# Kernel tuning notes

Hardware: AMD Instinct MI355X
Metric: run time of the kernel (lower is better)

## Reference

```python
import jax, jax.numpy as jnp
import numpy as np

DA, DZ, HID, IM = 5, 10, 128, 64


def _encode(x, w1, b1, w2, b2, w3, b3, wd, bd):
    # Conv2D k=4 s=2 'same' (pad 1,1) + ReLU, x3, then flatten + Dense(20)
    dn = ('NHWC', 'HWIO', 'NHWC')
    for w, b in ((w1, b1), (w2, b2), (w3, b3)):
        x = jax.lax.conv_general_dilated(x, w, (2, 2), [(1, 1), (1, 1)], dimension_numbers=dn)
        x = jax.nn.relu(x + b)
    x = x.reshape(x.shape[0], -1)
    return x @ wd + bd


def _lstm(a_in, k, rk, b):
    # keras LSTM, gate order i,f,c,o; stateful step-by-step == scan over shifted seq
    B = a_in.shape[0]
    def step(carry, x):
        h, c = carry
        g = x @ k + h @ rk + b
        gi, gf, gg, go = jnp.split(g, 4, axis=-1)
        c = jax.nn.sigmoid(gf) * c + jax.nn.sigmoid(gi) * jnp.tanh(gg)
        h = jax.nn.sigmoid(go) * jnp.tanh(c)
        return (h, c), h
    z = jnp.zeros((B, HID), a_in.dtype)
    _, hs = jax.lax.scan(step, (z, z), jnp.swapaxes(a_in, 0, 1))
    return hs  # [T, B, HID]


def _forward(images, w1, b1, w2, b2, w3, b3, wd, bd, lk, lrk, lb, wabc, babc):
    B, T = images.shape[0], images.shape[1]
    # encode all frames in one batched pass (per-frame encode is recursion-independent)
    lat = _encode(images.reshape(B * T, IM, IM, 1), w1, b1, w2, b2, w3, b3, wd, bd)
    a_all = lat[:, :DA].reshape(B, T, DA)  # encode() mean split
    # LSTM consumes a_prev: a0=zeros at t=0, then a_{t-1}
    a_in = jnp.concatenate([jnp.zeros((B, 1, DA), a_all.dtype), a_all[:, :-1]], axis=1)
    hs = _lstm(a_in, lk, lrk, lb)  # [T,B,HID]
    abc = hs @ wabc + babc  # [T,B,DZ*DZ+DA*DZ]
    A = abc[..., :DZ * DZ].reshape(T, B, DZ, DZ)
    C = abc[..., DZ * DZ:].reshape(T, B, DA, DZ)

    Q = 0.08 * jnp.eye(DZ, dtype=a_all.dtype)
    R = 0.03 * jnp.eye(DA, dtype=a_all.dtype)
    I = jnp.eye(DZ, dtype=a_all.dtype)
    std_min = 1e-4 * I

    def kf(carry, inp):
        z, P = carry
        At, Ct, at = inp
        z_hat = jnp.einsum('bij,bj->bi', At, z)
        P_hat = At @ P @ jnp.swapaxes(At, -1, -2) + Q
        resid = at - jnp.einsum('bij,bj->bi', Ct, z_hat)
        S = Ct @ P_hat @ jnp.swapaxes(Ct, -1, -2) + R
        K = P_hat @ jnp.swapaxes(Ct, -1, -2) @ jnp.linalg.inv(S)
        pz = z_hat + jnp.einsum('bij,bj->bi', K, resid)
        pP = (I - K @ Ct) @ P_hat
        # note: clamped P_hat is stored, but update() above used the unclamped one
        return (pz, pP), (z_hat, jnp.maximum(P_hat, std_min), pz, pP)

    z0 = jnp.zeros((B, DZ), a_all.dtype)
    P0 = jnp.broadcast_to(I, (B, DZ, DZ))
    _, (z_hat_s, P_hat_s, pz_s, pP_s) = jax.lax.scan(kf, (z0, P0), (A, C, jnp.swapaxes(a_all, 0, 1)))
    last_z, last_P = pz_s[-1], pP_s[-1]

    def rts(carry, inp):
        zs, Ps = carry
        pz_prev, pP_prev, Aj, zhj, Phj = inp
        D = pP_prev @ jnp.swapaxes(Aj, -1, -2) @ jnp.linalg.inv(Phj)
        zn = pz_prev + jnp.einsum('bij,bj->bi', D, zs - zhj)
        Pn = pP_prev + D @ (Ps - Phj) @ jnp.swapaxes(D, -1, -2)
        return (zn, Pn), (zn, Pn)

    # j = T-1 .. 1, reading post[j-1], A[j], z_hat[j], P_hat_clamped[j]
    rev = (pz_s[:-1][::-1], pP_s[:-1][::-1], A[1:][::-1], z_hat_s[1:][::-1], P_hat_s[1:][::-1])
    _, (zsm_r, Psm_r) = jax.lax.scan(rts, (last_z, last_P), rev)
    z_smooth = jnp.swapaxes(zsm_r[::-1], 0, 1)  # [B, T-1, DZ]
    P_smooth = jnp.swapaxes(Psm_r[::-1], 0, 1)  # [B, T-1, DZ, DZ]
    return z_smooth, P_smooth, a_all, A, C, last_z, last_P


def setup_inputs() -> dict:
    key = jax.random.key(0)
    ks = jax.random.split(key, 9)
    B, T = 3, 128
    f = lambda k, shape, s: jax.random.normal(k, shape, jnp.float32) * s
    return {
        'images': jax.random.uniform(ks[0], (B, T, IM, IM, 1), jnp.float32),
        'w1': f(ks[1], (4, 4, 1, 64), 0.25), 'b1': jnp.zeros((64,), jnp.float32),
        'w2': f(ks[2], (4, 4, 64, 128), 0.03), 'b2': jnp.zeros((128,), jnp.float32),
        'w3': f(ks[3], (4, 4, 128, 512), 0.022), 'b3': jnp.zeros((512,), jnp.float32),
        'wd': f(ks[4], (8 * 8 * 512, 20), 0.006), 'bd': jnp.zeros((20,), jnp.float32),
        'lk': f(ks[5], (DA, 4 * HID), 0.3), 'lrk': f(ks[6], (HID, 4 * HID), 0.08),
        'lb': jnp.zeros((4 * HID,), jnp.float32),
        'wabc': f(ks[7], (HID, DZ * DZ + DA * DZ), 0.02),
        'babc': jnp.zeros((DZ * DZ + DA * DZ,), jnp.float32),
    }


def reference(images, w1, b1, w2, b2, w3, b3, wd, bd, lk, lrk, lb, wabc, babc):
    return _forward(images, w1, b1, w2, b2, w3, b3, wd, bd, lk, lrk, lb, wabc, babc)
```

## Files before the change

kernel.cpp:

```cpp
#include <hip/hip_runtime.h>
#include <math.h>

typedef unsigned int   u32;
typedef unsigned short u16;
typedef short bf16x8 __attribute__((ext_vector_type(8)));
typedef float f32x4  __attribute__((ext_vector_type(4)));

#define OUT_ZS    0
#define OUT_PS    3810
#define OUT_AALL  41910
#define OUT_A     43830
#define OUT_C     82230
#define OUT_LASTZ 101430
#define OUT_LASTP 101460

__device__ __forceinline__ float sigm(float x){ return 1.f/(1.f+expf(-x)); }
__device__ __forceinline__ float safed(float d){
    return (fabsf(d) < 1e-30f) ? ((d < 0.f) ? -1e-30f : 1e-30f) : d;
}
__device__ __forceinline__ u16 f2b(float f) {
    union { float f; u32 u; } v; v.f = f;
    u32 r = v.u + 0x7fffu + ((v.u >> 16) & 1u);
    return (u16)(r >> 16);
}
__device__ __forceinline__ float b2f(u16 u) {
    union { u32 x; float f; } v; v.x = ((u32)u) << 16; return v.f;
}
__device__ __forceinline__ u32 packb(float a, float b){ return (u32)f2b(a) | ((u32)f2b(b) << 16); }

__device__ u16   r14_c1[25165824];
__device__ u16   r14_c2[12582912];
__device__ float r14_c3[12582912];
__device__ u16   r14_w2h[131072];
__device__ u16   r14_w2l[131072];
__device__ u16   r14_w3h[1048576];
__device__ u16   r14_w3l[1048576];
__device__ float r14_wdT[163840];
__device__ float r14_hs[49152];
__device__ float r14_zhat[3840];
__device__ float r14_phat[38400];
__device__ float r14_pz[3840];
__device__ float r14_pp[38400];
__device__ float r14_aall[1920];
__device__ float r14_A[38400];
__device__ float r14_C[19200];
__device__ float r14_G[38400];

__global__ __launch_bounds__(256) void conv1_r14(const float* __restrict__ img,
        const float* __restrict__ w1, const float* __restrict__ b1, u16* __restrict__ out)
{
    __shared__ float in_lds[66*66];
    const int f = blockIdx.x, tid = threadIdx.x;
    const int og = tid >> 5, sg = tid & 31;

    for (int i = tid; i < 66*66; i += 256) in_lds[i] = 0.f;
    __syncthreads();
    const float4* src = (const float4*)(img + f*4096);
    for (int i = tid; i < 1024; i += 256) {
        int r = i >> 4, c0 = (i & 15) * 4;
        float4 v = src[i];
        float* dst = &in_lds[(r+1)*66 + c0 + 1];
        dst[0]=v.x; dst[1]=v.y; dst[2]=v.z; dst[3]=v.w;
    }
    float wr[16][8];
    #pragma unroll
    for (int k = 0; k < 16; k++) {
        float4 a = *(const float4*)&w1[k*64 + og*8];
        float4 b = *(const float4*)&w1[k*64 + og*8 + 4];
        wr[k][0]=a.x; wr[k][1]=a.y; wr[k][2]=a.z; wr[k][3]=a.w;
        wr[k][4]=b.x; wr[k][5]=b.y; wr[k][6]=b.z; wr[k][7]=b.w;
    }
    float bias[8];
    #pragma unroll
    for (int j = 0; j < 8; j++) bias[j] = b1[og*8+j];
    __syncthreads();

    for (int yy = 0; yy < 32; yy++) {
        float inv[16];
        #pragma unroll
        for (int ky = 0; ky < 4; ky++)
            #pragma unroll
            for (int kx = 0; kx < 4; kx++)
                inv[ky*4+kx] = in_lds[(2*yy+ky)*66 + 2*sg+kx];
        float acc[8];
        #pragma unroll
        for (int j = 0; j < 8; j++) acc[j] = bias[j];
        #pragma unroll
        for (int k = 0; k < 16; k++)
            #pragma unroll
            for (int j = 0; j < 8; j++) acc[j] += inv[k]*wr[k][j];
        #pragma unroll
        for (int j = 0; j < 8; j++) acc[j] = fmaxf(acc[j], 0.f);
        uint4 pk = make_uint4(packb(acc[0],acc[1]), packb(acc[2],acc[3]),
                              packb(acc[4],acc[5]), packb(acc[6],acc[7]));
        *(uint4*)(out + (f*1024 + yy*32 + sg)*64 + og*8) = pk;
    }
}

__global__ __launch_bounds__(256) void w2t_r14(const float* __restrict__ w2,
        u16* __restrict__ hi, u16* __restrict__ lo)
{
    int idx = blockIdx.x*256 + threadIdx.x;
    if (idx < 131072) {
        int k = idx >> 7, oc = idx & 127;
        float v = w2[idx];
        u16 h = f2b(v);
        hi[oc*1024 + k] = h;
        lo[oc*1024 + k] = f2b(v - b2f(h));
    }
}
__global__ __launch_bounds__(256) void w3t_r14(const float* __restrict__ w3,
        u16* __restrict__ hi, u16* __restrict__ lo)
{
    int idx = blockIdx.x*256 + threadIdx.x;
    if (idx < 1048576) {
        int k = idx >> 9, oc = idx & 511;
        float v = w3[idx];
        u16 h = f2b(v);
        hi[oc*2048 + k] = h;
        lo[oc*2048 + k] = f2b(v - b2f(h));
    }
}
__global__ __launch_bounds__(256) void wdt_r14(const float* __restrict__ wd, float* __restrict__ wdT)
{
    int idx = blockIdx.x*256 + threadIdx.x;
    if (idx < 163840) {
        int j = idx & 32767, d = idx >> 15;
        wdT[d*32768 + j] = wd[j*20 + d];
    }
}

__global__ __launch_bounds__(256) void conv2_r14(const u16* __restrict__ c1b,
        const u16* __restrict__ w2h, const u16* __restrict__ w2l,
        const float* __restrict__ b2, u16* __restrict__ c2b)
{
    __shared__ __align__(16) u16 slab[128*72];
    const int f = blockIdx.x, mc = blockIdx.y, tid = threadIdx.x;
    const int wave = tid >> 6, lane = tid & 63, quad = lane >> 4, ln = lane & 15;

    f32x4 acc[8][2];
    const f32x4 zz = {0.f, 0.f, 0.f, 0.f};
    #pragma unroll
    for (int mt = 0; mt < 8; mt++) { acc[mt][0] = zz; acc[mt][1] = zz; }

    const int sp = tid >> 1;
    const int sy = mc*8 + (sp >> 4), sx = sp & 15;
    const int sic = (tid & 1) * 32;

    for (int kk = 0; kk < 16; kk++) {
        const int ky = kk >> 2, kx = kk & 3;
        __syncthreads();
        {
            int iy = 2*sy - 1 + ky, ix = 2*sx - 1 + kx;
            uint4* d4 = (uint4*)&slab[sp*72 + sic];
            if (iy >= 0 && iy < 32 && ix >= 0 && ix < 32) {
                const uint4* s4 = (const uint4*)&c1b[((f*32 + iy)*32 + ix)*64 + sic];
                d4[0]=s4[0]; d4[1]=s4[1]; d4[2]=s4[2]; d4[3]=s4[3];
            } else {
                uint4 z = make_uint4(0,0,0,0);
                d4[0]=z; d4[1]=z; d4[2]=z; d4[3]=z;
            }
        }
        __syncthreads();
        #pragma unroll
        for (int ks = 0; ks < 2; ks++) {
            bf16x8 af[8];
            #pragma unroll
            for (int mt = 0; mt < 8; mt++)
                af[mt] = *(const bf16x8*)&slab[(mt*16 + ln)*72 + ks*32 + quad*8];
            #pragma unroll
            for (int nt = 0; nt < 2; nt++) {
                const int oc = wave*32 + nt*16 + ln;
                const int kb = kk*64 + ks*32 + quad*8;
                bf16x8 bh = *(const bf16x8*)&w2h[oc*1024 + kb];
                bf16x8 bl = *(const bf16x8*)&w2l[oc*1024 + kb];
                #pragma unroll
                for (int mt = 0; mt < 8; mt++) {
                    acc[mt][nt] = __builtin_amdgcn_mfma_f32_16x16x32_bf16(af[mt], bh, acc[mt][nt], 0,0,0);
                    acc[mt][nt] = __builtin_amdgcn_mfma_f32_16x16x32_bf16(af[mt], bl, acc[mt][nt], 0,0,0);
                }
            }
        }
    }
    #pragma unroll
    for (int nt = 0; nt < 2; nt++) {
        const int oc = wave*32 + nt*16 + ln;
        const float bias = b2[oc];
        #pragma unroll
        for (int mt = 0; mt < 8; mt++)
            #pragma unroll
            for (int r = 0; r < 4; r++) {
                int pix = mc*128 + mt*16 + quad*4 + r;
                c2b[(f*256 + pix)*128 + oc] = f2b(fmaxf(acc[mt][nt][r] + bias, 0.f));
            }
    }
}

__global__ __launch_bounds__(256) void conv3_r14(const u16* __restrict__ c2b,
        const u16* __restrict__ w3h, const u16* __restrict__ w3l,
        const float* __restrict__ b3, float* __restrict__ c3)
{
    __shared__ __align__(16) u16 slab[64*136];
    const int f = blockIdx.x, ocg = blockIdx.y, tid = threadIdx.x;
    const int wave = tid >> 6, lane = tid & 63, quad = lane >> 4, ln = lane & 15;
    const int wn = ocg*256 + wave*64;

    f32x4 acc[4][4];
    const f32x4 zz = {0.f, 0.f, 0.f, 0.f};
    #pragma unroll
    for (int mt = 0; mt < 4; mt++)
        #pragma unroll
        for (int nt = 0; nt < 4; nt++) acc[mt][nt] = zz;

    const int sp = tid >> 2;
    const int sy = sp >> 3, sx = sp & 7;
    const int sic = (tid & 3) * 32;

    for (int kk = 0; kk < 16; kk++) {
        const int ky = kk >> 2, kx = kk & 3;
        __syncthreads();
        {
            int iy = 2*sy - 1 + ky, ix = 2*sx - 1 + kx;
            uint4* d4 = (uint4*)&slab[sp*136 + sic];
            if (iy >= 0 && iy < 16 && ix >= 0 && ix < 16) {
                const uint4* s4 = (const uint4*)&c2b[((f*16 + iy)*16 + ix)*128 + sic];
                d4[0]=s4[0]; d4[1]=s4[1]; d4[2]=s4[2]; d4[3]=s4[3];
            } else {
                uint4 z = make_uint4(0,0,0,0);
                d4[0]=z; d4[1]=z; d4[2]=z; d4[3]=z;
            }
        }
        __syncthreads();
        #pragma unroll
        for (int ks = 0; ks < 4; ks++) {
            bf16x8 af[4];
            #pragma unroll
            for (int mt = 0; mt < 4; mt++)
                af[mt] = *(const bf16x8*)&slab[(mt*16 + ln)*136 + ks*32 + quad*8];
            #pragma unroll
            for (int nt = 0; nt < 4; nt++) {
                const int oc = wn + nt*16 + ln;
                const int kb = kk*128 + ks*32 + quad*8;
                bf16x8 bh = *(const bf16x8*)&w3h[oc*2048 + kb];
                bf16x8 bl = *(const bf16x8*)&w3l[oc*2048 + kb];
                #pragma unroll
                for (int mt = 0; mt < 4; mt++) {
                    acc[mt][nt] = __builtin_amdgcn_mfma_f32_16x16x32_bf16(af[mt], bh, acc[mt][nt], 0,0,0);
                    acc[mt][nt] = __builtin_amdgcn_mfma_f32_16x16x32_bf16(af[mt], bl, acc[mt][nt], 0,0,0);
                }
            }
        }
    }
    #pragma unroll
    for (int nt = 0; nt < 4; nt++) {
        const int oc = wn + nt*16 + ln;
        const float bias = b3[oc];
        #pragma unroll
        for (int mt = 0; mt < 4; mt++)
            #pragma unroll
            for (int r = 0; r < 4; r++) {
                int pix = mt*16 + quad*4 + r;
                c3[(f*64 + pix)*512 + oc] = fmaxf(acc[mt][nt][r] + bias, 0.f);
            }
    }
}

__global__ __launch_bounds__(256) void dense_r14(const float* __restrict__ bd,
        float* __restrict__ dout)
{
    const int f = blockIdx.x, tid = threadIdx.x;
    float p0=0,p1=0,p2=0,p3=0,p4=0;
    const float4* x4 = (const float4*)(r14_c3 + f*32768);
    for (int j = tid; j < 8192; j += 256) {
        float4 v = x4[j];
        float4 w0 = *(const float4*)&r14_wdT[          4*j];
        float4 w1 = *(const float4*)&r14_wdT[32768   + 4*j];
        float4 w2 = *(const float4*)&r14_wdT[65536   + 4*j];
        float4 w3 = *(const float4*)&r14_wdT[98304   + 4*j];
        float4 w4 = *(const float4*)&r14_wdT[131072  + 4*j];
        p0 += v.x*w0.x + v.y*w0.y + v.z*w0.z + v.w*w0.w;
        p1 += v.x*w1.x + v.y*w1.y + v.z*w1.z + v.w*w1.w;
        p2 += v.x*w2.x + v.y*w2.y + v.z*w2.z + v.w*w2.w;
        p3 += v.x*w3.x + v.y*w3.y + v.z*w3.z + v.w*w3.w;
        p4 += v.x*w4.x + v.y*w4.y + v.z*w4.z + v.w*w4.w;
    }
    __shared__ float red[5][256];
    red[0][tid]=p0; red[1][tid]=p1; red[2][tid]=p2; red[3][tid]=p3; red[4][tid]=p4;
    __syncthreads();
    for (int st = 128; st > 0; st >>= 1) {
        if (tid < st) {
            #pragma unroll
            for (int d = 0; d < 5; d++) red[d][tid] += red[d][tid+st];
        }
        __syncthreads();
    }
    if (tid < 5) {
        float v = red[tid][0] + bd[tid];
        r14_aall[f*5 + tid] = v;
        dout[OUT_AALL + f*5 + tid] = v;
    }
}

__global__ __launch_bounds__(512) void lstm_r14(const float* __restrict__ lk,
        const float* __restrict__ lrk, const float* __restrict__ lb)
{
    const int b = blockIdx.x, c = threadIdx.x;
    __shared__ float a_lds[640];
    __shared__ float h_lds[128];
    __shared__ float g_lds[512];
    for (int i = c; i < 640; i += 512) a_lds[i] = r14_aall[b*640 + i];
    if (c < 128) h_lds[c] = 0.f;
    float wreg[128];
    #pragma unroll
    for (int j = 0; j < 128; j++) wreg[j] = lrk[j*512 + c];
    float lkr[5];
    #pragma unroll
    for (int d = 0; d < 5; d++) lkr[d] = lk[d*512 + c];
    const float gb = lb[c];
    float cs = 0.f;
    __syncthreads();
    for (int t = 0; t < 128; t++) {
        float g = gb;
        if (t > 0) {
            #pragma unroll
            for (int d = 0; d < 5; d++) g += a_lds[(t-1)*5 + d] * lkr[d];
        }
        float s0=0.f, s1=0.f, s2=0.f, s3=0.f;
        #pragma unroll
        for (int j = 0; j < 128; j += 4) {
            float4 h4 = *(const float4*)&h_lds[j];
            s0 += h4.x*wreg[j];   s1 += h4.y*wreg[j+1];
            s2 += h4.z*wreg[j+2]; s3 += h4.w*wreg[j+3];
        }
        g += (s0 + s1) + (s2 + s3);
        g_lds[c] = g;
        __syncthreads();
        if (c < 128) {
            float gi = g_lds[c], gf = g_lds[c+128], gg = g_lds[c+256], go = g_lds[c+384];
            cs = sigm(gf)*cs + sigm(gi)*tanhf(gg);
            float hn = sigm(go)*tanhf(cs);
            h_lds[c] = hn;
            r14_hs[(t*3 + b)*128 + c] = hn;
        }
        __syncthreads();
    }
}

__global__ __launch_bounds__(192) void abc_r14(const float* __restrict__ wabc,
        const float* __restrict__ babc, float* __restrict__ dout)
{
    const int tb = blockIdx.x, c = threadIdx.x;
    __shared__ float h_lds[128];
    if (c < 128) h_lds[c] = r14_hs[tb*128 + c];
    __syncthreads();
    if (c < 150) {
        float s = babc[c];
        for (int j = 0; j < 128; j++) s += h_lds[j]*wabc[j*150 + c];
        if (c < 100) { r14_A[tb*100 + c] = s; dout[OUT_A + tb*100 + c] = s; }
        else         { r14_C[tb*50 + (c-100)] = s; dout[OUT_C + tb*50 + (c-100)] = s; }
    }
}

__global__ __launch_bounds__(128) void kf_r15(float* __restrict__ dout)
{
    const int b = blockIdx.x, tid = threadIdx.x;
    const int i10 = tid/10, j10 = tid%10;
    __shared__ float Ab[2][100], Cb[2][56], avb[2][8];
    __shared__ float z[12], P[100], zh[12], AP[100], Ph[100], resid[8],
                     CPm[52], PCt[52], Ssh[28], Kg[52];

    float rA = 0.f, rC = 0.f, rav = 0.f;
    if (tid < 100) rA  = r14_A[(0*3+b)*100 + tid];
    if (tid < 50)  rC  = r14_C[(0*3+b)*50 + tid];
    if (tid < 5)   rav = r14_aall[(b*128+0)*5 + tid];
    if (tid < 100) P[tid] = (i10==j10) ? 1.f : 0.f;
    if (tid < 10)  z[tid] = 0.f;
    if (tid < 100) Ab[0][tid] = rA;
    if (tid < 50)  Cb[0][tid] = rC;
    if (tid < 5)   avb[0][tid] = rav;
    if (tid < 100) rA  = r14_A[(1*3+b)*100 + tid];
    if (tid < 50)  rC  = r14_C[(1*3+b)*50 + tid];
    if (tid < 5)   rav = r14_aall[(b*128+1)*5 + tid];
    __syncthreads();

    for (int t = 0; t < 128; t++) {
        const int cb = t & 1, nb = cb ^ 1;
        const float* Ax = Ab[cb];
        const float* Cx = Cb[cb];

        if (tid < 100) {
            float s = 0.f;
            #pragma unroll
            for (int k = 0; k < 10; k++) s += Ax[i10*10+k]*P[k*10+j10];
            AP[tid] = s;
        } else if (tid < 110) {
            const int i = tid - 100;
            float s = 0.f;
            #pragma unroll
            for (int k = 0; k < 10; k++) s += Ax[i*10+k]*z[k];
            zh[i] = s;
        }
        __syncthreads();

        if (tid < 100) {
            float s = (i10==j10) ? 0.08f : 0.f;
            #pragma unroll
            for (int k = 0; k < 10; k++) s += AP[i10*10+k]*Ax[j10*10+k];
            Ph[tid] = s;
        } else if (tid < 105) {
            const int c = tid - 100;
            float s = avb[cb][c];
            #pragma unroll
            for (int k = 0; k < 10; k++) s -= Cx[c*10+k]*zh[k];
            resid[c] = s;
        }
        __syncthreads();

        if (tid < 50) {
            const int i = tid/10, j = tid%10;
            float s = 0.f;
            #pragma unroll
            for (int k = 0; k < 10; k++) s += Cx[i*10+k]*Ph[k*10+j];
            CPm[tid] = s;
        } else if (tid >= 64 && tid < 114) {
            const int q = tid-64, i = q/5, j = q%5;
            float s = 0.f;
            #pragma unroll
            for (int k = 0; k < 10; k++) s += Ph[i*10+k]*Cx[j*10+k];
            PCt[q] = s;
        }
        __syncthreads();

        if (tid < 25) {
            const int i = tid/5, j = tid%5;
            float s = (i==j) ? 0.03f : 0.f;
            #pragma unroll
            for (int k = 0; k < 10; k++) s += CPm[i*10+k]*Cx[j*10+k];
            Ssh[tid] = s;
        }
        __syncthreads();

        if (tid < 10) {
            float M[5][5], bb[5], pv[5], x[5];
            #pragma unroll
            for (int r = 0; r < 5; r++)
                #pragma unroll
                for (int c = 0; c < 5; c++) M[r][c] = Ssh[c*5+r];
            #pragma unroll
            for (int k = 0; k < 5; k++) bb[k] = PCt[tid*5+k];
            #pragma unroll
            for (int k = 0; k < 5; k++) {
                const float p = 1.f/safed(M[k][k]);
                pv[k] = p;
                #pragma unroll
                for (int r = k+1; r < 5; r++) {
                    const float f = M[r][k]*p;
                    #pragma unroll
                    for (int c = k+1; c < 5; c++) M[r][c] -= f*M[k][c];
                    bb[r] -= f*bb[k];
                }
            }
            #pragma unroll
            for (int k = 4; k >= 0; k--) {
                float s = bb[k];
                #pragma unroll
                for (int c = k+1; c < 5; c++) s -= M[k][c]*x[c];
                x[k] = s*pv[k];
            }
            #pragma unroll
            for (int k = 0; k < 5; k++) Kg[tid*5+k] = x[k];
        }
        __syncthreads();

        if (tid < 100) {
            float s = Ph[tid];
            #pragma unroll
            for (int k = 0; k < 5; k++) s -= Kg[i10*5+k]*CPm[k*10+j10];
            r14_pp[(t*3+b)*100 + tid] = s;
            P[tid] = s;
            r14_phat[(t*3+b)*100 + tid] = fmaxf(Ph[tid], (i10==j10)?1e-4f:0.f);
            if (tid < 10) r14_zhat[(t*3+b)*10 + tid] = zh[tid];
        } else if (tid < 110) {
            const int i = tid - 100;
            float s = zh[i];
            #pragma unroll
            for (int k = 0; k < 5; k++) s += Kg[i*5+k]*resid[k];
            r14_pz[(t*3+b)*10 + i] = s;
            z[i] = s;
        }
        if (t < 127) {
            if (tid < 100) Ab[nb][tid] = rA;
            if (tid < 50)  Cb[nb][tid] = rC;
            if (tid < 5)   avb[nb][tid] = rav;
            if (t < 126) {
                if (tid < 100) rA  = r14_A[((t+2)*3+b)*100 + tid];
                if (tid < 50)  rC  = r14_C[((t+2)*3+b)*50 + tid];
                if (tid < 5)   rav = r14_aall[(b*128+(t+2))*5 + tid];
            }
        }
        __syncthreads();
    }
    if (tid < 10)  dout[OUT_LASTZ + b*10 + tid]  = z[tid];
    if (tid < 100) dout[OUT_LASTP + b*100 + tid] = P[tid];
}

__global__ __launch_bounds__(256) void ginv_r14()
{
    const int idx = blockIdx.x;
    const int tt = idx/3 + 1, b = idx%3;
    const int tid = threadIdx.x;
    __shared__ float M[10][21];
    __shared__ float A[100];
    __shared__ int piv;
    if (tid < 100) {
        int i = tid/10, j = tid%10;
        M[i][j] = r14_phat[(tt*3+b)*100 + tid];
        M[i][10+j] = (i==j) ? 1.f : 0.f;
        A[tid] = r14_A[(tt*3+b)*100 + tid];
    }
    __syncthreads();
    const int r = tid/20, cc = tid%20;
    for (int k = 0; k < 10; k++) {
        if (tid == 0) {
            int p = k; float best = fabsf(M[k][k]);
            for (int rr = k+1; rr < 10; rr++) {
                float v = fabsf(M[rr][k]);
                if (v > best) { best = v; p = rr; }
            }
            piv = p;
        }
        __syncthreads();
        if (piv != k && tid < 20) {
            float a = M[k][tid], bb = M[piv][tid];
            M[k][tid] = bb; M[piv][tid] = a;
        }
        __syncthreads();
        float pinv = 1.f/safed(M[k][k]);
        float myf = 0.f, rowv = 0.f;
        if (tid < 200) { myf = M[r][k]; rowv = M[k][cc]; }
        __syncthreads();
        if (tid < 200) {
            if (r == k) M[k][cc] = rowv*pinv;
            else        M[r][cc] -= myf*pinv*rowv;
        }
        __syncthreads();
    }
    if (tid < 100) {
        int i = tid/10, j = tid%10;
        float s = 0.f;
        #pragma unroll
        for (int k = 0; k < 10; k++) s += A[k*10+i]*M[k][10+j];
        r14_G[(tt*3+b)*100 + tid] = s;
    }
}

__global__ __launch_bounds__(128) void rts_r14(float* __restrict__ dout)
{
    const int b = blockIdx.x, tid = threadIdx.x;
    const int i10 = tid/10, j10 = tid%10;
    __shared__ float zc[10], Pc[100], D[100], Gt[100], pPm[100], ph[100],
                     zh[10], pzv[10], dz[10], T1[100], zn[10], Pnn[100];
    if (tid < 10)  zc[tid] = r14_pz[(127*3+b)*10 + tid];
    if (tid < 100) Pc[tid] = r14_pp[(127*3+b)*100 + tid];
    for (int t = 126; t >= 0; t--) {
        __syncthreads();
        if (tid < 100) {
            Gt[tid]  = r14_G[((t+1)*3+b)*100 + tid];
            pPm[tid] = r14_pp[(t*3+b)*100 + tid];
            ph[tid]  = r14_phat[((t+1)*3+b)*100 + tid];
        }
        if (tid < 10) {
            zh[tid]  = r14_zhat[((t+1)*3+b)*10 + tid];
            pzv[tid] = r14_pz[(t*3+b)*10 + tid];
        }
        __syncthreads();
        if (tid < 100){ float s=0.f; for (int k=0;k<10;k++) s += pPm[i10*10+k]*Gt[k*10+j10]; D[tid]=s; }
        if (tid < 10) dz[tid] = zc[tid] - zh[tid];
        __syncthreads();
        if (tid < 10) { float s=pzv[tid]; for (int k=0;k<10;k++) s += D[tid*10+k]*dz[k]; zn[tid]=s; }
        if (tid < 100){ float s=0.f; for (int k=0;k<10;k++) s += D[i10*10+k]*(Pc[k*10+j10]-ph[k*10+j10]); T1[tid]=s; }
        __syncthreads();
        if (tid < 100){ float s=pPm[tid]; for (int k=0;k<10;k++) s += T1[i10*10+k]*D[j10*10+k]; Pnn[tid]=s; }
        __syncthreads();
        if (tid < 10) { dout[OUT_ZS + (b*127+t)*10 + tid] = zn[tid]; zc[tid]=zn[tid]; }
        if (tid < 100){ dout[OUT_PS + (b*127+t)*100 + tid] = Pnn[tid]; Pc[tid]=Pnn[tid]; }
    }
}

extern "C" void kernel_launch(void* const* d_in, const int* in_sizes, int n_in,
                              void* d_out, int out_size, void* d_ws, size_t ws_size,
                              hipStream_t stream)
{
    (void)in_sizes; (void)n_in; (void)out_size; (void)d_ws; (void)ws_size;
    const float* images = (const float*)d_in[0];
    const float* w1   = (const float*)d_in[1];
    const float* b1   = (const float*)d_in[2];
    const float* w2   = (const float*)d_in[3];
    const float* b2   = (const float*)d_in[4];
    const float* w3   = (const float*)d_in[5];
    const float* b3   = (const float*)d_in[6];
    const float* wd   = (const float*)d_in[7];
    const float* bd   = (const float*)d_in[8];
    const float* lk   = (const float*)d_in[9];
    const float* lrk  = (const float*)d_in[10];
    const float* lb   = (const float*)d_in[11];
    const float* wabc = (const float*)d_in[12];
    const float* babc = (const float*)d_in[13];
    float* dout = (float*)d_out;

    u16 *c1p, *c2p, *w2hp, *w2lp, *w3hp, *w3lp;
    float *c3p, *wdTp;
    hipGetSymbolAddress((void**)&c1p,  HIP_SYMBOL(r14_c1));
    hipGetSymbolAddress((void**)&c2p,  HIP_SYMBOL(r14_c2));
    hipGetSymbolAddress((void**)&c3p,  HIP_SYMBOL(r14_c3));
    hipGetSymbolAddress((void**)&w2hp, HIP_SYMBOL(r14_w2h));
    hipGetSymbolAddress((void**)&w2lp, HIP_SYMBOL(r14_w2l));
    hipGetSymbolAddress((void**)&w3hp, HIP_SYMBOL(r14_w3h));
    hipGetSymbolAddress((void**)&w3lp, HIP_SYMBOL(r14_w3l));
    hipGetSymbolAddress((void**)&wdTp, HIP_SYMBOL(r14_wdT));

    conv1_r14<<<dim3(384), dim3(256), 0, stream>>>(images, w1, b1, c1p);
    w2t_r14<<<dim3(512), dim3(256), 0, stream>>>(w2, w2hp, w2lp);
    w3t_r14<<<dim3(4096), dim3(256), 0, stream>>>(w3, w3hp, w3lp);
    wdt_r14<<<dim3(640), dim3(256), 0, stream>>>(wd, wdTp);
    conv2_r14<<<dim3(384, 2), dim3(256), 0, stream>>>(c1p, w2hp, w2lp, b2, c2p);
    conv3_r14<<<dim3(384, 2), dim3(256), 0, stream>>>(c2p, w3hp, w3lp, b3, c3p);
    dense_r14<<<dim3(384), dim3(256), 0, stream>>>(bd, dout);
    lstm_r14<<<dim3(3), dim3(512), 0, stream>>>(lk, lrk, lb);
    abc_r14<<<dim3(384), dim3(192), 0, stream>>>(wabc, babc, dout);
    kf_r15<<<dim3(3), dim3(128), 0, stream>>>(dout);
    ginv_r14<<<dim3(381), dim3(256), 0, stream>>>();
    rts_r14<<<dim3(3), dim3(128), 0, stream>>>(dout);
}
```

Baseline: 1.008 ms.

## Stage full input rows per ky in conv2/conv3 to reuse across kx taps

Restructures the conv2 and conv3 implicit-GEMM loops so that each ky iteration loads a whole strip of input rows into shared memory once, and all four kx taps index into it. Padding columns point at a zeroed sentinel row. This cuts the number of global-to-LDS staging passes and barriers from 16 to 4 per block. In exchange it uses larger LDS tiles, which may lower occupancy, and computes shared-memory addresses per lane.

Measured after the change: 1.078 ms. 6.9% more time.

```diff
diff --git a/kernel.cpp b/kernel.cpp
--- a/kernel.cpp
+++ b/kernel.cpp
@@ -130,11 +130,11 @@
     }
 }
 
-__global__ __launch_bounds__(256) void conv2_r14(const u16* __restrict__ c1b,
+__global__ __launch_bounds__(256) void conv2_r16(const u16* __restrict__ c1b,
         const u16* __restrict__ w2h, const u16* __restrict__ w2l,
         const float* __restrict__ b2, u16* __restrict__ c2b)
 {
-    __shared__ __align__(16) u16 slab[128*72];
+    __shared__ __align__(16) u16 tile[257*72];
     const int f = blockIdx.x, mc = blockIdx.y, tid = threadIdx.x;
     const int wave = tid >> 6, lane = tid & 63, quad = lane >> 4, ln = lane & 15;
 
@@ -143,41 +143,45 @@
     #pragma unroll
     for (int mt = 0; mt < 8; mt++) { acc[mt][0] = zz; acc[mt][1] = zz; }
 
-    const int sp = tid >> 1;
-    const int sy = mc*8 + (sp >> 4), sx = sp & 15;
-    const int sic = (tid & 1) * 32;
-
-    for (int kk = 0; kk < 16; kk++) {
-        const int ky = kk >> 2, kx = kk & 3;
-        __syncthreads();
-        {
-            int iy = 2*sy - 1 + ky, ix = 2*sx - 1 + kx;
-            uint4* d4 = (uint4*)&slab[sp*72 + sic];
-            if (iy >= 0 && iy < 32 && ix >= 0 && ix < 32) {
-                const uint4* s4 = (const uint4*)&c1b[((f*32 + iy)*32 + ix)*64 + sic];
-                d4[0]=s4[0]; d4[1]=s4[1]; d4[2]=s4[2]; d4[3]=s4[3];
-            } else {
-                uint4 z = make_uint4(0,0,0,0);
-                d4[0]=z; d4[1]=z; d4[2]=z; d4[3]=z;
-            }
-        }
-        __syncthreads();
-        #pragma unroll
-        for (int ks = 0; ks < 2; ks++) {
-            bf16x8 af[8];
-            #pragma unroll
-            for (int mt = 0; mt < 8; mt++)
-                af[mt] = *(const bf16x8*)&slab[(mt*16 + ln)*72 + ks*32 + quad*8];
-            #pragma unroll
-            for (int nt = 0; nt < 2; nt++) {
-                const int oc = wave*32 + nt*16 + ln;
-                const int kb = kk*64 + ks*32 + quad*8;
-                bf16x8 bh = *(const bf16x8*)&w2h[oc*1024 + kb];
-                bf16x8 bl = *(const bf16x8*)&w2l[oc*1024 + kb];
+    if (tid < 9) *(uint4*)&tile[256*72 + tid*8] = make_uint4(0,0,0,0);
+
+    for (int ky = 0; ky < 4; ky++) {
+        __syncthreads();
+        #pragma unroll
+        for (int i = 0; i < 8; i++) {
+            const int q = tid + 256*i;
+            const int slot = q >> 3, j = q & 7;
+            const int syl = slot >> 5, sx = slot & 31;
+            const int iy = 2*(mc*8 + syl) - 1 + ky;
+            uint4 v = make_uint4(0,0,0,0);
+            if ((unsigned)iy < 32u)
+                v = *(const uint4*)&c1b[((f*32 + iy)*32 + sx)*64 + j*8];
+            *(uint4*)&tile[slot*72 + j*8] = v;
+        }
+        __syncthreads();
+        #pragma unroll
+        for (int kx = 0; kx < 4; kx++) {
+            const int ix = 2*ln - 1 + kx;
+            const bool vx = (unsigned)ix < 32u;
+            const int kbb = (ky*4 + kx)*64 + quad*8;
+            #pragma unroll
+            for (int ks = 0; ks < 2; ks++) {
+                bf16x8 af[8];
                 #pragma unroll
                 for (int mt = 0; mt < 8; mt++) {
-                    acc[mt][nt] = __builtin_amdgcn_mfma_f32_16x16x32_bf16(af[mt], bh, acc[mt][nt], 0,0,0);
-                    acc[mt][nt] = __builtin_amdgcn_mfma_f32_16x16x32_bf16(af[mt], bl, acc[mt][nt], 0,0,0);
+                    const int slot = vx ? (mt*32 + ix) : 256;
+                    af[mt] = *(const bf16x8*)&tile[slot*72 + ks*32 + quad*8];
+                }
+                #pragma unroll
+                for (int nt = 0; nt < 2; nt++) {
+                    const int oc = wave*32 + nt*16 + ln;
+                    bf16x8 bh = *(const bf16x8*)&w2h[oc*1024 + kbb + ks*32];
+                    bf16x8 bl = *(const bf16x8*)&w2l[oc*1024 + kbb + ks*32];
+                    #pragma unroll
+                    for (int mt = 0; mt < 8; mt++) {
+                        acc[mt][nt] = __builtin_amdgcn_mfma_f32_16x16x32_bf16(af[mt], bh, acc[mt][nt], 0,0,0);
+                        acc[mt][nt] = __builtin_amdgcn_mfma_f32_16x16x32_bf16(af[mt], bl, acc[mt][nt], 0,0,0);
+                    }
                 }
             }
         }
@@ -196,14 +200,18 @@
     }
 }
 
-__global__ __launch_bounds__(256) void conv3_r14(const u16* __restrict__ c2b,
+__global__ __launch_bounds__(256) void conv3_r16(const u16* __restrict__ c2b,
         const u16* __restrict__ w3h, const u16* __restrict__ w3l,
         const float* __restrict__ b3, float* __restrict__ c3)
 {
-    __shared__ __align__(16) u16 slab[64*136];
+    __shared__ __align__(16) u16 tile[129*136];
     const int f = blockIdx.x, ocg = blockIdx.y, tid = threadIdx.x;
     const int wave = tid >> 6, lane = tid & 63, quad = lane >> 4, ln = lane & 15;
     const int wn = ocg*256 + wave*64;
+    const int px = ln & 7;
+    int pyv[4];
+    #pragma unroll
+    for (int mt = 0; mt < 4; mt++) pyv[mt] = mt*2 + (ln >> 3);
 
     f32x4 acc[4][4];
     const f32x4 zz = {0.f, 0.f, 0.f, 0.f};
@@ -212,41 +220,49 @@
         #pragma unroll
         for (int nt = 0; nt < 4; nt++) acc[mt][nt] = zz;
 
-    const int sp = tid >> 2;
-    const int sy = sp >> 3, sx = sp & 7;
-    const int sic = (tid & 3) * 32;
-
-    for (int kk = 0; kk < 16; kk++) {
-        const int ky = kk >> 2, kx = kk & 3;
-        __syncthreads();
-        {
-            int iy = 2*sy - 1 + ky, ix = 2*sx - 1 + kx;
-            uint4* d4 = (uint4*)&slab[sp*136 + sic];
-            if (iy >= 0 && iy < 16 && ix >= 0 && ix < 16) {
-                const uint4* s4 = (const uint4*)&c2b[((f*16 + iy)*16 + ix)*128 + sic];
-                d4[0]=s4[0]; d4[1]=s4[1]; d4[2]=s4[2]; d4[3]=s4[3];
-            } else {
-                uint4 z = make_uint4(0,0,0,0);
-                d4[0]=z; d4[1]=z; d4[2]=z; d4[3]=z;
-            }
-        }
-        __syncthreads();
-        #pragma unroll
-        for (int ks = 0; ks < 4; ks++) {
-            bf16x8 af[4];
-            #pragma unroll
-            for (int mt = 0; mt < 4; mt++)
-                af[mt] = *(const bf16x8*)&slab[(mt*16 + ln)*136 + ks*32 + quad*8];
-            #pragma unroll
-            for (int nt = 0; nt < 4; nt++) {
-                const int oc = wn + nt*16 + ln;
-                const int kb = kk*128 + ks*32 + quad*8;
-                bf16x8 bh = *(const bf16x8*)&w3h[oc*2048 + kb];
-                bf16x8 bl = *(const bf16x8*)&w3l[oc*2048 + kb];
+    if (tid < 17) *(uint4*)&tile[128*136 + tid*8] = make_uint4(0,0,0,0);
+
+    for (int ky = 0; ky < 4; ky++) {
+        __syncthreads();
+        #pragma unroll
+        for (int i = 0; i < 8; i++) {
+            const int q = tid + 256*i;
+            const int slot = q >> 4, j = q & 15;
+            const int sy = slot >> 4, sx = slot & 15;
+            const int iy = 2*sy - 1 + ky;
+            uint4 v = make_uint4(0,0,0,0);
+            if ((unsigned)iy < 16u)
+                v = *(const uint4*)&c2b[((f*16 + iy)*16 + sx)*128 + j*8];
+            *(uint4*)&tile[slot*136 + j*8] = v;
+        }
+        __syncthreads();
+        #pragma unroll
+        for (int kx = 0; kx < 4; kx++) {
+            const int ix = 2*px - 1 + kx;
+            const bool vx = (unsigned)ix < 16u;
+            int sa[4];
+            #pragma unroll
+            for (int mt = 0; mt < 4; mt++) {
+                const int slot = vx ? (pyv[mt]*16 + ix) : 128;
+                sa[mt] = slot*136 + quad*8;
+            }
+            const int kbb = (ky*4 + kx)*128 + quad*8;
+            #pragma unroll
+            for (int ks = 0; ks < 4; ks++) {
+                bf16x8 af[4];
                 #pragma unroll
-                for (int mt = 0; mt < 4; mt++) {
-                    acc[mt][nt] = __builtin_amdgcn_mfma_f32_16x16x32_bf16(af[mt], bh, acc[mt][nt], 0,0,0);
-                    acc[mt][nt] = __builtin_amdgcn_mfma_f32_16x16x32_bf16(af[mt], bl, acc[mt][nt], 0,0,0);
+                for (int mt = 0; mt < 4; mt++)
+                    af[mt] = *(const bf16x8*)&tile[sa[mt] + ks*32];
+                #pragma unroll
+                for (int nt = 0; nt < 4; nt++) {
+                    const int oc = wn + nt*16 + ln;
+                    bf16x8 bh = *(const bf16x8*)&w3h[oc*2048 + kbb + ks*32];
+                    bf16x8 bl = *(const bf16x8*)&w3l[oc*2048 + kbb + ks*32];
+                    #pragma unroll
+                    for (int mt = 0; mt < 4; mt++) {
+                        acc[mt][nt] = __builtin_amdgcn_mfma_f32_16x16x32_bf16(af[mt], bh, acc[mt][nt], 0,0,0);
+                        acc[mt][nt] = __builtin_amdgcn_mfma_f32_16x16x32_bf16(af[mt], bl, acc[mt][nt], 0,0,0);
+                    }
                 }
             }
         }
@@ -623,8 +639,8 @@
     w2t_r14<<<dim3(512), dim3(256), 0, stream>>>(w2, w2hp, w2lp);
     w3t_r14<<<dim3(4096), dim3(256), 0, stream>>>(w3, w3hp, w3lp);
     wdt_r14<<<dim3(640), dim3(256), 0, stream>>>(wd, wdTp);
-    conv2_r14<<<dim3(384, 2), dim3(256), 0, stream>>>(c1p, w2hp, w2lp, b2, c2p);
-    conv3_r14<<<dim3(384, 2), dim3(256), 0, stream>>>(c2p, w3hp, w3lp, b3, c3p);
+    conv2_r16<<<dim3(384, 2), dim3(256), 0, stream>>>(c1p, w2hp, w2lp, b2, c2p);
+    conv3_r16<<<dim3(384, 2), dim3(256), 0, stream>>>(c2p, w3hp, w3lp, b3, c3p);
     dense_r14<<<dim3(384), dim3(256), 0, stream>>>(bd, dout);
     lstm_r14<<<dim3(3), dim3(512), 0, stream>>>(lk, lrk, lb);
     abc_r14<<<dim3(384), dim3(192), 0, stream>>>(wabc, babc, dout);
```

## Stage input halo tiles once per channel half in conv2/conv3 instead of per-tap im2col

Applied to the files above, without the earlier changes.

Conv2 and conv3 used to rebuild an im2col slab in LDS for each of the 16 kernel taps, with two barriers per tap and repeated global reads of overlapping input pixels. They now load the whole input region once per channel half: a 10-row halo for conv2, the full 16x16 frame for conv3. Each tap's A fragments are then gathered straight from that tile, with padding masked in registers. This removes most barriers and redundant global loads. Conv2 also drops from 128 to 64 pixels per block and uses 4 row-blocks per frame, which doubles the weight fragment reloads per output, and the grid order is swapped so frames sit on y.

Result: slower. 1.108 ms (+9.9%).

```diff
diff --git a/kernel.cpp b/kernel.cpp
--- a/kernel.cpp
+++ b/kernel.cpp
@@ -130,119 +130,55 @@
     }
 }
 
-__global__ __launch_bounds__(256) void conv2_r14(const u16* __restrict__ c1b,
+__global__ __launch_bounds__(256) void conv2_r19(const u16* __restrict__ c1b,
         const u16* __restrict__ w2h, const u16* __restrict__ w2l,
         const float* __restrict__ b2, u16* __restrict__ c2b)
 {
-    __shared__ __align__(16) u16 slab[128*72];
-    const int f = blockIdx.x, mc = blockIdx.y, tid = threadIdx.x;
+    __shared__ __align__(16) u16 tile[320*36];
+    const int qy = blockIdx.x, f = blockIdx.y, tid = threadIdx.x;
     const int wave = tid >> 6, lane = tid & 63, quad = lane >> 4, ln = lane & 15;
-
-    f32x4 acc[8][2];
+    const int y0 = qy*4;
+
+    f32x4 acc[4][2];
     const f32x4 zz = {0.f, 0.f, 0.f, 0.f};
     #pragma unroll
-    for (int mt = 0; mt < 8; mt++) { acc[mt][0] = zz; acc[mt][1] = zz; }
-
-    const int sp = tid >> 1;
-    const int sy = mc*8 + (sp >> 4), sx = sp & 15;
-    const int sic = (tid & 1) * 32;
-
-    for (int kk = 0; kk < 16; kk++) {
-        const int ky = kk >> 2, kx = kk & 3;
-        __syncthreads();
-        {
-            int iy = 2*sy - 1 + ky, ix = 2*sx - 1 + kx;
-            uint4* d4 = (uint4*)&slab[sp*72 + sic];
-            if (iy >= 0 && iy < 32 && ix >= 0 && ix < 32) {
-                const uint4* s4 = (const uint4*)&c1b[((f*32 + iy)*32 + ix)*64 + sic];
-                d4[0]=s4[0]; d4[1]=s4[1]; d4[2]=s4[2]; d4[3]=s4[3];
-            } else {
-                uint4 z = make_uint4(0,0,0,0);
-                d4[0]=z; d4[1]=z; d4[2]=z; d4[3]=z;
-            }
-        }
-        __syncthreads();
-        #pragma unroll
-        for (int ks = 0; ks < 2; ks++) {
-            bf16x8 af[8];
-            #pragma unroll
-            for (int mt = 0; mt < 8; mt++)
-                af[mt] = *(const bf16x8*)&slab[(mt*16 + ln)*72 + ks*32 + quad*8];
+    for (int mt = 0; mt < 4; mt++) { acc[mt][0] = zz; acc[mt][1] = zz; }
+
+    const bf16x8 z8 = {0,0,0,0,0,0,0,0};
+
+    for (int ich = 0; ich < 2; ich++) {
+        if (ich) __syncthreads();
+        #pragma unroll
+        for (int i = 0; i < 5; i++) {
+            const int q = i*256 + tid;
+            const int s = q >> 2, ch = q & 3;
+            const int r = s >> 5, ix = s & 31;
+            const int iy = 2*y0 - 1 + r;
+            uint4 v = make_uint4(0,0,0,0);
+            if ((unsigned)iy < 32u)
+                v = *(const uint4*)&c1b[((f*32 + iy)*32 + ix)*64 + ich*32 + ch*8];
+            *(uint4*)&tile[s*36 + ch*8] = v;
+        }
+        __syncthreads();
+
+        #pragma unroll 4
+        for (int kk = 0; kk < 16; kk++) {
+            const int ky = kk >> 2, kx = kk & 3;
+            const int ix = 2*ln - 1 + kx;
+            const bool vx = (unsigned)ix < 32u;
+            bf16x8 af[4];
+            #pragma unroll
+            for (int mt = 0; mt < 4; mt++) {
+                const int s = (2*mt + ky)*32 + (ix & 31);
+                bf16x8 v = *(const bf16x8*)&tile[s*36 + quad*8];
+                af[mt] = vx ? v : z8;
+            }
+            const int kb = kk*64 + ich*32 + quad*8;
             #pragma unroll
             for (int nt = 0; nt < 2; nt++) {
                 const int oc = wave*32 + nt*16 + ln;
-                const int kb = kk*64 + ks*32 + quad*8;
                 bf16x8 bh = *(const bf16x8*)&w2h[oc*1024 + kb];
                 bf16x8 bl = *(const bf16x8*)&w2l[oc*1024 + kb];
-                #pragma unroll
-                for (int mt = 0; mt < 8; mt++) {
-                    acc[mt][nt] = __builtin_amdgcn_mfma_f32_16x16x32_bf16(af[mt], bh, acc[mt][nt], 0,0,0);
-                    acc[mt][nt] = __builtin_amdgcn_mfma_f32_16x16x32_bf16(af[mt], bl, acc[mt][nt], 0,0,0);
-                }
-            }
-        }
-    }
-    #pragma unroll
-    for (int nt = 0; nt < 2; nt++) {
-        const int oc = wave*32 + nt*16 + ln;
-        const float bias = b2[oc];
-        #pragma unroll
-        for (int mt = 0; mt < 8; mt++)
-            #pragma unroll
-            for (int r = 0; r < 4; r++) {
-                int pix = mc*128 + mt*16 + quad*4 + r;
-                c2b[(f*256 + pix)*128 + oc] = f2b(fmaxf(acc[mt][nt][r] + bias, 0.f));
-            }
-    }
-}
-
-__global__ __launch_bounds__(256) void conv3_r14(const u16* __restrict__ c2b,
-        const u16* __restrict__ w3h, const u16* __restrict__ w3l,
-        const float* __restrict__ b3, float* __restrict__ c3)
-{
-    __shared__ __align__(16) u16 slab[64*136];
-    const int f = blockIdx.x, ocg = blockIdx.y, tid = threadIdx.x;
-    const int wave = tid >> 6, lane = tid & 63, quad = lane >> 4, ln = lane & 15;
-    const int wn = ocg*256 + wave*64;
-
-    f32x4 acc[4][4];
-    const f32x4 zz = {0.f, 0.f, 0.f, 0.f};
-    #pragma unroll
-    for (int mt = 0; mt < 4; mt++)
-        #pragma unroll
-        for (int nt = 0; nt < 4; nt++) acc[mt][nt] = zz;
-
-    const int sp = tid >> 2;
-    const int sy = sp >> 3, sx = sp & 7;
-    const int sic = (tid & 3) * 32;
-
-    for (int kk = 0; kk < 16; kk++) {
-        const int ky = kk >> 2, kx = kk & 3;
-        __syncthreads();
-        {
-            int iy = 2*sy - 1 + ky, ix = 2*sx - 1 + kx;
-            uint4* d4 = (uint4*)&slab[sp*136 + sic];
-            if (iy >= 0 && iy < 16 && ix >= 0 && ix < 16) {
-                const uint4* s4 = (const uint4*)&c2b[((f*16 + iy)*16 + ix)*128 + sic];
-                d4[0]=s4[0]; d4[1]=s4[1]; d4[2]=s4[2]; d4[3]=s4[3];
-            } else {
-                uint4 z = make_uint4(0,0,0,0);
-                d4[0]=z; d4[1]=z; d4[2]=z; d4[3]=z;
-            }
-        }
-        __syncthreads();
-        #pragma unroll
-        for (int ks = 0; ks < 4; ks++) {
-            bf16x8 af[4];
-            #pragma unroll
-            for (int mt = 0; mt < 4; mt++)
-                af[mt] = *(const bf16x8*)&slab[(mt*16 + ln)*136 + ks*32 + quad*8];
-            #pragma unroll
-            for (int nt = 0; nt < 4; nt++) {
-                const int oc = wn + nt*16 + ln;
-                const int kb = kk*128 + ks*32 + quad*8;
-                bf16x8 bh = *(const bf16x8*)&w3h[oc*2048 + kb];
-                bf16x8 bl = *(const bf16x8*)&w3l[oc*2048 + kb];
                 #pragma unroll
                 for (int mt = 0; mt < 4; mt++) {
                     acc[mt][nt] = __builtin_amdgcn_mfma_f32_16x16x32_bf16(af[mt], bh, acc[mt][nt], 0,0,0);
@@ -251,6 +187,88 @@
             }
         }
     }
+
+    #pragma unroll
+    for (int nt = 0; nt < 2; nt++) {
+        const int oc = wave*32 + nt*16 + ln;
+        const float bias = b2[oc];
+        #pragma unroll
+        for (int mt = 0; mt < 4; mt++)
+            #pragma unroll
+            for (int r = 0; r < 4; r++) {
+                const int pix = (y0 + mt)*16 + quad*4 + r;
+                c2b[(f*256 + pix)*128 + oc] = f2b(fmaxf(acc[mt][nt][r] + bias, 0.f));
+            }
+    }
+}
+
+__global__ __launch_bounds__(256) void conv3_r19(const u16* __restrict__ c2b,
+        const u16* __restrict__ w3h, const u16* __restrict__ w3l,
+        const float* __restrict__ b3, float* __restrict__ c3)
+{
+    __shared__ __align__(16) u16 tile[256*72];
+    const int ocg = blockIdx.x, f = blockIdx.y, tid = threadIdx.x;
+    const int wave = tid >> 6, lane = tid & 63, quad = lane >> 4, ln = lane & 15;
+    const int wn = ocg*256 + wave*64;
+    const int px = ln & 7, lyb = ln >> 3;
+
+    f32x4 acc[4][4];
+    const f32x4 zz = {0.f, 0.f, 0.f, 0.f};
+    #pragma unroll
+    for (int mt = 0; mt < 4; mt++)
+        #pragma unroll
+        for (int nt = 0; nt < 4; nt++) acc[mt][nt] = zz;
+
+    const bf16x8 z8 = {0,0,0,0,0,0,0,0};
+
+    for (int ich = 0; ich < 2; ich++) {
+        if (ich) __syncthreads();
+        #pragma unroll
+        for (int i = 0; i < 8; i++) {
+            const int q = i*256 + tid;
+            const int s = q >> 3, ch = q & 7;
+            uint4 v = *(const uint4*)&c2b[(f*256 + s)*128 + ich*64 + ch*8];
+            *(uint4*)&tile[s*72 + ch*8] = v;
+        }
+        __syncthreads();
+
+        #pragma unroll 4
+        for (int kk = 0; kk < 16; kk++) {
+            const int ky = kk >> 2, kx = kk & 3;
+            const int ix = 2*px - 1 + kx;
+            const bool vx = (unsigned)ix < 16u;
+            int sbase[4]; bool vm[4];
+            #pragma unroll
+            for (int mt = 0; mt < 4; mt++) {
+                const int ly = 2*mt + lyb;
+                const int iy = 2*ly - 1 + ky;
+                vm[mt] = vx && ((unsigned)iy < 16u);
+                sbase[mt] = ((iy & 15)*16 + (ix & 15))*72;
+            }
+            #pragma unroll
+            for (int ks = 0; ks < 2; ks++) {
+                bf16x8 af[4];
+                #pragma unroll
+                for (int mt = 0; mt < 4; mt++) {
+                    bf16x8 v = *(const bf16x8*)&tile[sbase[mt] + (ks*4 + quad)*8];
+                    af[mt] = vm[mt] ? v : z8;
+                }
+                const int kb = kk*128 + ich*64 + ks*32 + quad*8;
+                #pragma unroll
+                for (int nt = 0; nt < 4; nt++) {
+                    const int oc = wn + nt*16 + ln;
+                    bf16x8 bh = *(const bf16x8*)&w3h[oc*2048 + kb];
+                    bf16x8 bl = *(const bf16x8*)&w3l[oc*2048 + kb];
+                    #pragma unroll
+                    for (int mt = 0; mt < 4; mt++) {
+                        acc[mt][nt] = __builtin_amdgcn_mfma_f32_16x16x32_bf16(af[mt], bh, acc[mt][nt], 0,0,0);
+                        acc[mt][nt] = __builtin_amdgcn_mfma_f32_16x16x32_bf16(af[mt], bl, acc[mt][nt], 0,0,0);
+                    }
+                }
+            }
+        }
+    }
+
     #pragma unroll
     for (int nt = 0; nt < 4; nt++) {
         const int oc = wn + nt*16 + ln;
@@ -259,7 +277,7 @@
         for (int mt = 0; mt < 4; mt++)
             #pragma unroll
             for (int r = 0; r < 4; r++) {
-                int pix = mt*16 + quad*4 + r;
+                const int pix = mt*16 + quad*4 + r;
                 c3[(f*64 + pix)*512 + oc] = fmaxf(acc[mt][nt][r] + bias, 0.f);
             }
     }
@@ -623,8 +641,8 @@
     w2t_r14<<<dim3(512), dim3(256), 0, stream>>>(w2, w2hp, w2lp);
     w3t_r14<<<dim3(4096), dim3(256), 0, stream>>>(w3, w3hp, w3lp);
     wdt_r14<<<dim3(640), dim3(256), 0, stream>>>(wd, wdTp);
-    conv2_r14<<<dim3(384, 2), dim3(256), 0, stream>>>(c1p, w2hp, w2lp, b2, c2p);
-    conv3_r14<<<dim3(384, 2), dim3(256), 0, stream>>>(c2p, w3hp, w3lp, b3, c3p);
+    conv2_r19<<<dim3(4, 384), dim3(256), 0, stream>>>(c1p, w2hp, w2lp, b2, c2p);
+    conv3_r19<<<dim3(2, 384), dim3(256), 0, stream>>>(c2p, w3hp, w3lp, b3, c3p);
     dense_r14<<<dim3(384), dim3(256), 0, stream>>>(bd, dout);
     lstm_r14<<<dim3(3), dim3(512), 0, stream>>>(lk, lrk, lb);
     abc_r14<<<dim3(384), dim3(192), 0, stream>>>(wabc, babc, dout);
```

## Fuse dense projection into conv3 epilogue and bias-combine inside LSTM

Applied to the files above, without the earlier changes.

Conv3 now multiplies its ReLU outputs directly by the dense weights in its epilogue, reduces five partial sums per block in LDS, and writes per-(frame, oc-group) partials. The LSTM kernel adds the two partials and the bias to form a_all. This removes the 50MB fp32 c3 intermediate write and re-read, the wd transpose kernel and the separate dense kernel. The cost is strided 20-float weight reads per output element in the epilogue and an extra LDS reduction in conv3.

Result: slower. 1.036 ms (+2.8%).

```diff
diff --git a/kernel.cpp b/kernel.cpp
--- a/kernel.cpp
+++ b/kernel.cpp
@@ -30,12 +30,11 @@
 
 __device__ u16   r14_c1[25165824];
 __device__ u16   r14_c2[12582912];
-__device__ float r14_c3[12582912];
 __device__ u16   r14_w2h[131072];
 __device__ u16   r14_w2l[131072];
 __device__ u16   r14_w3h[1048576];
 __device__ u16   r14_w3l[1048576];
-__device__ float r14_wdT[163840];
+__device__ float r20_dpart[3840];
 __device__ float r14_hs[49152];
 __device__ float r14_zhat[3840];
 __device__ float r14_phat[38400];
@@ -119,14 +118,6 @@
         u16 h = f2b(v);
         hi[oc*2048 + k] = h;
         lo[oc*2048 + k] = f2b(v - b2f(h));
-    }
-}
-__global__ __launch_bounds__(256) void wdt_r14(const float* __restrict__ wd, float* __restrict__ wdT)
-{
-    int idx = blockIdx.x*256 + threadIdx.x;
-    if (idx < 163840) {
-        int j = idx & 32767, d = idx >> 15;
-        wdT[d*32768 + j] = wd[j*20 + d];
     }
 }
 
@@ -196,9 +187,9 @@
     }
 }
 
-__global__ __launch_bounds__(256) void conv3_r14(const u16* __restrict__ c2b,
+__global__ __launch_bounds__(256) void conv3_r20(const u16* __restrict__ c2b,
         const u16* __restrict__ w3h, const u16* __restrict__ w3l,
-        const float* __restrict__ b3, float* __restrict__ c3)
+        const float* __restrict__ b3, const float* __restrict__ wd)
 {
     __shared__ __align__(16) u16 slab[64*136];
     const int f = blockIdx.x, ocg = blockIdx.y, tid = threadIdx.x;
@@ -251,6 +242,8 @@
             }
         }
     }
+
+    float pd0=0.f, pd1=0.f, pd2=0.f, pd3=0.f, pd4=0.f;
     #pragma unroll
     for (int nt = 0; nt < 4; nt++) {
         const int oc = wn + nt*16 + ln;
@@ -259,56 +252,44 @@
         for (int mt = 0; mt < 4; mt++)
             #pragma unroll
             for (int r = 0; r < 4; r++) {
-                int pix = mt*16 + quad*4 + r;
-                c3[(f*64 + pix)*512 + oc] = fmaxf(acc[mt][nt][r] + bias, 0.f);
-            }
-    }
-}
-
-__global__ __launch_bounds__(256) void dense_r14(const float* __restrict__ bd,
-        float* __restrict__ dout)
-{
-    const int f = blockIdx.x, tid = threadIdx.x;
-    float p0=0,p1=0,p2=0,p3=0,p4=0;
-    const float4* x4 = (const float4*)(r14_c3 + f*32768);
-    for (int j = tid; j < 8192; j += 256) {
-        float4 v = x4[j];
-        float4 w0 = *(const float4*)&r14_wdT[          4*j];
-        float4 w1 = *(const float4*)&r14_wdT[32768   + 4*j];
-        float4 w2 = *(const float4*)&r14_wdT[65536   + 4*j];
-        float4 w3 = *(const float4*)&r14_wdT[98304   + 4*j];
-        float4 w4 = *(const float4*)&r14_wdT[131072  + 4*j];
-        p0 += v.x*w0.x + v.y*w0.y + v.z*w0.z + v.w*w0.w;
-        p1 += v.x*w1.x + v.y*w1.y + v.z*w1.z + v.w*w1.w;
-        p2 += v.x*w2.x + v.y*w2.y + v.z*w2.z + v.w*w2.w;
-        p3 += v.x*w3.x + v.y*w3.y + v.z*w3.z + v.w*w3.w;
-        p4 += v.x*w4.x + v.y*w4.y + v.z*w4.z + v.w*w4.w;
-    }
-    __shared__ float red[5][256];
-    red[0][tid]=p0; red[1][tid]=p1; red[2][tid]=p2; red[3][tid]=p3; red[4][tid]=p4;
+                const int pix = mt*16 + quad*4 + r;
+                const float v = fmaxf(acc[mt][nt][r] + bias, 0.f);
+                const float* wp = &wd[(pix*512 + oc)*20];
+                float4 w4 = *(const float4*)wp;
+                pd0 += v*w4.x; pd1 += v*w4.y; pd2 += v*w4.z; pd3 += v*w4.w;
+                pd4 += v*wp[4];
+            }
+    }
+    __syncthreads();
+    float* red = (float*)slab;
+    red[0*256+tid]=pd0; red[1*256+tid]=pd1; red[2*256+tid]=pd2;
+    red[3*256+tid]=pd3; red[4*256+tid]=pd4;
     __syncthreads();
     for (int st = 128; st > 0; st >>= 1) {
         if (tid < st) {
             #pragma unroll
-            for (int d = 0; d < 5; d++) red[d][tid] += red[d][tid+st];
-        }
-        __syncthreads();
-    }
-    if (tid < 5) {
-        float v = red[tid][0] + bd[tid];
-        r14_aall[f*5 + tid] = v;
-        dout[OUT_AALL + f*5 + tid] = v;
-    }
-}
-
-__global__ __launch_bounds__(512) void lstm_r14(const float* __restrict__ lk,
-        const float* __restrict__ lrk, const float* __restrict__ lb)
+            for (int d = 0; d < 5; d++) red[d*256+tid] += red[d*256+tid+st];
+        }
+        __syncthreads();
+    }
+    if (tid < 5) r20_dpart[(f*2 + ocg)*5 + tid] = red[tid*256];
+}
+
+__global__ __launch_bounds__(512) void lstm_r20(const float* __restrict__ lk,
+        const float* __restrict__ lrk, const float* __restrict__ lb,
+        const float* __restrict__ bd, float* __restrict__ dout)
 {
     const int b = blockIdx.x, c = threadIdx.x;
     __shared__ float a_lds[640];
     __shared__ float h_lds[128];
     __shared__ float g_lds[512];
-    for (int i = c; i < 640; i += 512) a_lds[i] = r14_aall[b*640 + i];
+    for (int i = c; i < 640; i += 512) {
+        const int f = b*128 + i/5, d = i % 5;
+        const float v = bd[d] + r20_dpart[f*10 + d] + r20_dpart[f*10 + 5 + d];
+        a_lds[i] = v;
+        r14_aall[f*5 + d] = v;
+        dout[OUT_AALL + f*5 + d] = v;
+    }
     if (c < 128) h_lds[c] = 0.f;
     float wreg[128];
     #pragma unroll
@@ -609,24 +590,19 @@
     float* dout = (float*)d_out;
 
     u16 *c1p, *c2p, *w2hp, *w2lp, *w3hp, *w3lp;
-    float *c3p, *wdTp;
     hipGetSymbolAddress((void**)&c1p,  HIP_SYMBOL(r14_c1));
     hipGetSymbolAddress((void**)&c2p,  HIP_SYMBOL(r14_c2));
-    hipGetSymbolAddress((void**)&c3p,  HIP_SYMBOL(r14_c3));
     hipGetSymbolAddress((void**)&w2hp, HIP_SYMBOL(r14_w2h));
     hipGetSymbolAddress((void**)&w2lp, HIP_SYMBOL(r14_w2l));
     hipGetSymbolAddress((void**)&w3hp, HIP_SYMBOL(r14_w3h));
     hipGetSymbolAddress((void**)&w3lp, HIP_SYMBOL(r14_w3l));
-    hipGetSymbolAddress((void**)&wdTp, HIP_SYMBOL(r14_wdT));
 
     conv1_r14<<<dim3(384), dim3(256), 0, stream>>>(images, w1, b1, c1p);
     w2t_r14<<<dim3(512), dim3(256), 0, stream>>>(w2, w2hp, w2lp);
     w3t_r14<<<dim3(4096), dim3(256), 0, stream>>>(w3, w3hp, w3lp);
-    wdt_r14<<<dim3(640), dim3(256), 0, stream>>>(wd, wdTp);
     conv2_r14<<<dim3(384, 2), dim3(256), 0, stream>>>(c1p, w2hp, w2lp, b2, c2p);
-    conv3_r14<<<dim3(384, 2), dim3(256), 0, stream>>>(c2p, w3hp, w3lp, b3, c3p);
-    dense_r14<<<dim3(384), dim3(256), 0, stream>>>(bd, dout);
-    lstm_r14<<<dim3(3), dim3(512), 0, stream>>>(lk, lrk, lb);
+    conv3_r20<<<dim3(384, 2), dim3(256), 0, stream>>>(c2p, w3hp, w3lp, b3, wd);
+    lstm_r20<<<dim3(3), dim3(512), 0, stream>>>(lk, lrk, lb, bd, dout);
     abc_r14<<<dim3(384), dim3(192), 0, stream>>>(wabc, babc, dout);
     kf_r15<<<dim3(3), dim3(128), 0, stream>>>(dout);
     ginv_r14<<<dim3(381), dim3(256), 0, stream>>>();
```
